# Optimization experiments

Hardware: AMD Instinct MI355X
Metric: run time of the kernel (lower is better)

Reference implementation:

```python
import jax, jax.numpy as jnp
import numpy as np

# Module config: RoDAlignMax(aligned_height=9, aligned_width=9, spatial_scale=0.25)
# Internally RoDAlignFunction is called with aligned_height+1, aligned_width+1,
# then max_pool2d(kernel=2, stride=1) shrinks each spatial dim by 1.
AH, AW = 10, 10          # pre-pool sampling grid (aligned_{h,w} + 1)
SPATIAL_SCALE = 0.25


def _rod_align(features, rois, ah, aw, scale):
    """RoDAlign: uniform bilinear sampling grid over the WHOLE feature map,
    with samples falling INSIDE the ROI zeroed out (region-of-discard).
    features: [B,C,H,W], rois: [R,5]=(batch_ind,x1,y1,x2,y2) -> [R,C,ah,aw]."""
    B, C, H, W = features.shape
    dt = features.dtype
    bidx = rois[:, 0].astype(jnp.int32)                              # [R]
    x1 = rois[:, 1] * scale
    y1 = rois[:, 2] * scale
    x2 = rois[:, 3] * scale
    y2 = rois[:, 4] * scale
    # uniform grid spanning the full feature map
    h = jnp.arange(ah, dtype=dt) * ((H - 1.0) / (ah - 1.0))          # [AH]
    w = jnp.arange(aw, dtype=dt) * ((W - 1.0) / (aw - 1.0))          # [AW]
    h0 = jnp.minimum(jnp.floor(h), H - 2).astype(jnp.int32)
    w0 = jnp.minimum(jnp.floor(w), W - 2).astype(jnp.int32)
    hr = (h - h0.astype(dt))[:, None, None]                          # [AH,1,1]
    wr = (w - w0.astype(dt))[None, :, None]                          # [1,AW,1]
    b = bidx[:, None, None]                                          # [R,1,1]
    hi0 = h0[None, :, None]; hi1 = hi0 + 1                           # [1,AH,1]
    wi0 = w0[None, None, :]; wi1 = wi0 + 1                           # [1,1,AW]
    # four corner gathers; advanced idx dims go first -> [R,AH,AW,C]
    ul = features[b, :, hi0, wi0]
    ur = features[b, :, hi0, wi1]
    dl = features[b, :, hi1, wi0]
    dr = features[b, :, hi1, wi1]
    out = (ul * (1 - hr) * (1 - wr) + ur * (1 - hr) * wr
           + dl * hr * (1 - wr) + dr * hr * wr)                      # [R,AH,AW,C]
    # zero samples inside the ROI (the kept crop region is discarded)
    in_h = (h[None, :] >= y1[:, None]) & (h[None, :] <= y2[:, None])  # [R,AH]
    in_w = (w[None, :] >= x1[:, None]) & (w[None, :] <= x2[:, None])  # [R,AW]
    inside = in_h[:, :, None] & in_w[:, None, :]                      # [R,AH,AW]
    out = jnp.where(inside[..., None], jnp.zeros((), dt), out)
    return jnp.transpose(out, (0, 3, 1, 2))                           # [R,C,AH,AW]


def _maxpool2x2_s1(x):
    # max_pool2d(kernel_size=2, stride=1) on [..., H, W]
    return jnp.maximum(jnp.maximum(x[..., :-1, :-1], x[..., :-1, 1:]),
                       jnp.maximum(x[..., 1:, :-1], x[..., 1:, 1:]))


def setup_inputs() -> dict:
    key = jax.random.key(0)
    k1, k2, k3, k4, k5 = jax.random.split(key, 5)
    B, C, H, W = 4, 256, 64, 64
    R = 2048
    img = H / SPATIAL_SCALE  # 256.0, input-image coordinate extent
    features = jax.random.normal(k1, (B, C, H, W), dtype=jnp.float32)
    bidx = jax.random.randint(k2, (R,), 0, B).astype(jnp.float32)
    x1 = jax.random.uniform(k3, (R,), dtype=jnp.float32) * (img * 0.5)
    y1 = jax.random.uniform(k4, (R,), dtype=jnp.float32) * (img * 0.5)
    wh = jax.random.uniform(k5, (R, 2), dtype=jnp.float32) * (img * 0.45) + img * 0.05
    x2 = jnp.minimum(x1 + wh[:, 0], img - 1.0)
    y2 = jnp.minimum(y1 + wh[:, 1], img - 1.0)
    rois = jnp.stack([bidx, x1, y1, x2, y2], axis=1)  # [R,5]
    return {"features": features, "rois": rois}


def reference(features, rois):
    x = _rod_align(features, rois, AH, AW, SPATIAL_SCALE)  # [R,C,10,10]
    return _maxpool2x2_s1(x)                               # [R,C,9,9]
```

## Files before the change

### kernel.cpp

```cpp
#include <hip/hip_runtime.h>


#define NB 4
#define NC 256
#define HW 64
#define NR 2048

__global__ __launch_bounds__(256) void rod_gather(const float* __restrict__ F,
                                                  float* __restrict__ G) {
    int idx = blockIdx.x * 256 + threadIdx.x;
    int c = idx & 255;
    int t = idx >> 8;
    int p = t % 100;
    int b = t / 100;
    int i = p / 10, j = p - i * 10;
    G[idx] = F[((b * NC + c) << 12) + i * 448 + j * 7];
}

__global__ __launch_bounds__(64) void rod_main(const float* __restrict__ G,
                                               const float* __restrict__ rois,
                                               float* __restrict__ out) {
    __shared__ __align__(16) float lds[64 * 81];
    const int tid = threadIdx.x;
    const int r   = blockIdx.x >> 2;
    const int q   = blockIdx.x & 3;
    const int c   = (q << 6) + tid;

    const float x1 = rois[r * 5 + 1] * 0.25f;
    const float y1 = rois[r * 5 + 2] * 0.25f;
    const float x2 = rois[r * 5 + 3] * 0.25f;
    const float y2 = rois[r * 5 + 4] * 0.25f;
    const int  b   = (int)rois[r * 5 + 0];

    bool inw[10], inh[10];
    #pragma unroll
    for (int j = 0; j < 10; ++j) {
        float s = 7.0f * (float)j;
        inw[j] = (s >= x1) && (s <= x2);
        inh[j] = (s >= y1) && (s <= y2);
    }

    const float* gb = G + (size_t)b * 100 * NC + c;

    float raw1[10];
    float vprev[10];
    {
        float raw0[10];
        #pragma unroll
        for (int j = 0; j < 10; ++j) raw0[j] = gb[j * NC];
        #pragma unroll
        for (int j = 0; j < 10; ++j) raw1[j] = gb[(10 + j) * NC];
        #pragma unroll
        for (int j = 0; j < 10; ++j) vprev[j] = (inh[0] && inw[j]) ? 0.0f : raw0[j];
    }

    #pragma unroll
    for (int i = 1; i < 10; ++i) {
        float rawn[10];
        if (i < 9) {
            #pragma unroll
            for (int j = 0; j < 10; ++j) rawn[j] = gb[((i + 1) * 10 + j) * NC];
        }
        float vcur[10];
        #pragma unroll
        for (int j = 0; j < 10; ++j) vcur[j] = (inh[i] && inw[j]) ? 0.0f : raw1[j];
        float rm[10];
        #pragma unroll
        for (int j = 0; j < 10; ++j) rm[j] = fmaxf(vprev[j], vcur[j]);
        #pragma unroll
        for (int j = 0; j < 9; ++j)
            lds[tid * 81 + (i - 1) * 9 + j] = fmaxf(rm[j], rm[j + 1]);
        #pragma unroll
        for (int j = 0; j < 10; ++j) vprev[j] = vcur[j];
        if (i < 9) {
            #pragma unroll
            for (int j = 0; j < 10; ++j) raw1[j] = rawn[j];
        }
    }
    __syncthreads();

    const float4* lds4 = reinterpret_cast<const float4*>(lds);
    float4* dst4 = reinterpret_cast<float4*>(out + (size_t)r * 20736 + q * 5184);
    #pragma unroll
    for (int k = 0; k < 20; ++k)
        dst4[tid + (k << 6)] = lds4[tid + (k << 6)];
    if (tid < 16)
        dst4[tid + 1280] = lds4[tid + 1280];
}

extern "C" void kernel_launch(void* const* d_in, const int* in_sizes, int n_in,
                              void* d_out, int out_size, void* d_ws, size_t ws_size,
                              hipStream_t stream) {
    const float* F    = (const float*)d_in[0];
    const float* rois = (const float*)d_in[1];
    float*       out  = (float*)d_out;
    float*       G    = (float*)d_ws;

    rod_gather<<<dim3(400), dim3(256), 0, stream>>>(F, G);
    rod_main<<<dim3(NR * 4), dim3(64), 0, stream>>>(G, rois, out);
}
```

Baseline: 178.3 us.

## Split ROI rows across half-waves and issue all gathers up front

Each 64-thread block now covers 32 channels instead of 64. The two half-waves take overlapping row bands (rows 0-5 and 4-9), and each produces its own slice of pooled output rows. The grid doubles, and each thread loads its 60 samples at once instead of streaming row by row, which is meant to raise memory-level parallelism and occupancy. In exchange, two input rows are loaded by both half-waves, and each block has a smaller LDS tile and a shorter copy-out.

Result: no change. 178.5 us (+0.1%).

```diff
diff --git a/kernel.cpp b/kernel.cpp
--- a/kernel.cpp
+++ b/kernel.cpp
@@ -17,14 +17,16 @@
     G[idx] = F[((b * NC + c) << 12) + i * 448 + j * 7];
 }
 
-__global__ __launch_bounds__(64) void rod_main(const float* __restrict__ G,
-                                               const float* __restrict__ rois,
-                                               float* __restrict__ out) {
-    __shared__ __align__(16) float lds[64 * 81];
-    const int tid = threadIdx.x;
-    const int r   = blockIdx.x >> 2;
-    const int q   = blockIdx.x & 3;
-    const int c   = (q << 6) + tid;
+__global__ __launch_bounds__(64, 2) void rod_main(const float* __restrict__ G,
+                                                  const float* __restrict__ rois,
+                                                  float* __restrict__ out) {
+    __shared__ __align__(16) float lds[32 * 81];
+    const int tid   = threadIdx.x;
+    const int r     = blockIdx.x >> 3;
+    const int oct   = blockIdx.x & 7;
+    const int cl    = tid & 31;
+    const int c     = (oct << 5) + cl;
+    const int rbase = (tid >> 5) << 2;
 
     const float x1 = rois[r * 5 + 1] * 0.25f;
     const float y1 = rois[r * 5 + 2] * 0.25f;
@@ -32,60 +34,58 @@
     const float y2 = rois[r * 5 + 4] * 0.25f;
     const int  b   = (int)rois[r * 5 + 0];
 
-    bool inw[10], inh[10];
+    bool inw[10];
     #pragma unroll
     for (int j = 0; j < 10; ++j) {
         float s = 7.0f * (float)j;
         inw[j] = (s >= x1) && (s <= x2);
-        inh[j] = (s >= y1) && (s <= y2);
+    }
+    bool inh[6];
+    #pragma unroll
+    for (int k = 0; k < 6; ++k) {
+        float s = 7.0f * (float)(rbase + k);
+        inh[k] = (s >= y1) && (s <= y2);
     }
 
     const float* gb = G + (size_t)b * 100 * NC + c;
 
-    float raw1[10];
-    float vprev[10];
-    {
-        float raw0[10];
+    float raw[6][10];
+    #pragma unroll
+    for (int k = 0; k < 6; ++k)
         #pragma unroll
-        for (int j = 0; j < 10; ++j) raw0[j] = gb[j * NC];
+        for (int j = 0; j < 10; ++j)
+            raw[k][j] = gb[((rbase + k) * 10 + j) * NC];
+
+    float m[6][10];
+    #pragma unroll
+    for (int k = 0; k < 6; ++k)
         #pragma unroll
-        for (int j = 0; j < 10; ++j) raw1[j] = gb[(10 + j) * NC];
+        for (int j = 0; j < 10; ++j)
+            m[k][j] = (inh[k] && inw[j]) ? 0.0f : raw[k][j];
+
+    float cm[5][10];
+    #pragma unroll
+    for (int k = 0; k < 5; ++k)
         #pragma unroll
-        for (int j = 0; j < 10; ++j) vprev[j] = (inh[0] && inw[j]) ? 0.0f : raw0[j];
-    }
+        for (int j = 0; j < 10; ++j)
+            cm[k][j] = fmaxf(m[k][j], m[k + 1][j]);
 
     #pragma unroll
-    for (int i = 1; i < 10; ++i) {
-        float rawn[10];
-        if (i < 9) {
-            #pragma unroll
-            for (int j = 0; j < 10; ++j) rawn[j] = gb[((i + 1) * 10 + j) * NC];
-        }
-        float vcur[10];
-        #pragma unroll
-        for (int j = 0; j < 10; ++j) vcur[j] = (inh[i] && inw[j]) ? 0.0f : raw1[j];
-        float rm[10];
-        #pragma unroll
-        for (int j = 0; j < 10; ++j) rm[j] = fmaxf(vprev[j], vcur[j]);
+    for (int k = 0; k < 5; ++k) {
+        if (k == 4 && rbase == 0) continue;
         #pragma unroll
         for (int j = 0; j < 9; ++j)
-            lds[tid * 81 + (i - 1) * 9 + j] = fmaxf(rm[j], rm[j + 1]);
-        #pragma unroll
-        for (int j = 0; j < 10; ++j) vprev[j] = vcur[j];
-        if (i < 9) {
-            #pragma unroll
-            for (int j = 0; j < 10; ++j) raw1[j] = rawn[j];
-        }
+            lds[cl * 81 + (rbase + k) * 9 + j] = fmaxf(cm[k][j], cm[k][j + 1]);
     }
     __syncthreads();
 
     const float4* lds4 = reinterpret_cast<const float4*>(lds);
-    float4* dst4 = reinterpret_cast<float4*>(out + (size_t)r * 20736 + q * 5184);
+    float4* dst4 = reinterpret_cast<float4*>(out + (size_t)r * 20736 + oct * 2592);
     #pragma unroll
-    for (int k = 0; k < 20; ++k)
+    for (int k = 0; k < 10; ++k)
         dst4[tid + (k << 6)] = lds4[tid + (k << 6)];
-    if (tid < 16)
-        dst4[tid + 1280] = lds4[tid + 1280];
+    if (tid < 8)
+        dst4[tid + 640] = lds4[tid + 640];
 }
 
 extern "C" void kernel_launch(void* const* d_in, const int* in_sizes, int n_in,
@@ -97,5 +97,5 @@
     float*       G    = (float*)d_ws;
 
     rod_gather<<<dim3(400), dim3(256), 0, stream>>>(F, G);
-    rod_main<<<dim3(NR * 4), dim3(64), 0, stream>>>(G, rois, out);
+    rod_main<<<dim3(NR * 8), dim3(64), 0, stream>>>(G, rois, out);
 }
```
